# Kernel tuning notes

Hardware: AMD Instinct MI355X
Metric: run time of the kernel (lower is better)

Reference implementation:

```python
import jax, jax.numpy as jnp
import numpy as np

B, T, I, H = 256, 512, 64, 256  # batch, seq_len, NUM_BANDS, HIDDEN_DIM; NUM_LAYERS=2


def setup_inputs() -> dict:
    key = jax.random.key(0)
    ks = jax.random.split(key, 12)
    s = 0.05
    f = jnp.float32
    return {
        "x": jax.random.normal(ks[0], (B, T, I), f),
        # layer 0 (input -> hidden)
        "W_ih0": jax.random.normal(ks[1], (H, I), f) * s,
        "W_hh0": jax.random.normal(ks[2], (H, H), f) * s,
        "b_ih0": jax.random.normal(ks[3], (H,), f) * s,
        "b_hh0": jax.random.normal(ks[4], (H,), f) * s,
        # layer 1 (hidden -> hidden)
        "W_ih1": jax.random.normal(ks[5], (H, H), f) * s,
        "W_hh1": jax.random.normal(ks[6], (H, H), f) * s,
        "b_ih1": jax.random.normal(ks[7], (H,), f) * s,
        "b_hh1": jax.random.normal(ks[8], (H,), f) * s,
        # fc head (hidden -> 1)
        "W_fc": jax.random.normal(ks[9], (1, H), f) * s,
        "b_fc": jax.random.normal(ks[10], (1,), f) * s,
    }


def _rnn_layer(x_seq, W_ih, W_hh, b_ih, b_hh):
    """Elman ReLU layer: h_t = relu(W_ih x_t + b_ih + W_hh h_{t-1} + b_hh).
    x_seq: [B, T, D] -> returns [B, T, H]. Input projection is batched; only
    the hidden recurrence runs in the scan."""
    pre = jnp.einsum('btd,hd->bth', x_seq, W_ih) + b_ih + b_hh  # [B,T,H]
    h0 = jnp.zeros((x_seq.shape[0], W_hh.shape[0]), x_seq.dtype)

    def step(h, p_t):
        h = jax.nn.relu(p_t + h @ W_hh.T)
        return h, h

    _, ys = jax.lax.scan(step, h0, jnp.swapaxes(pre, 0, 1))  # [T,B,H]
    return jnp.swapaxes(ys, 0, 1)


def reference(x, W_ih0, W_hh0, b_ih0, b_hh0, W_ih1, W_hh1, b_ih1, b_hh1, W_fc, b_fc):
    h1 = _rnn_layer(x, W_ih0, W_hh0, b_ih0, b_hh0)
    h2 = _rnn_layer(h1, W_ih1, W_hh1, b_ih1, b_hh1)
    out = h2.reshape(-1, h2.shape[-1]) @ W_fc.T + b_fc  # [B*T, 1]
    return out.reshape(-1)
```

## Files before the change

kernel.cpp:

```cpp
#include <hip/hip_runtime.h>


#define T_ 512
#define H_ 256

typedef __attribute__((ext_vector_type(8))) short short8;
typedef __attribute__((ext_vector_type(4))) float f32x4;

#define MFMA(a, b, c) __builtin_amdgcn_mfma_f32_16x16x32_bf16(a, b, c, 0, 0, 0)

__device__ __forceinline__ unsigned short bf16rne(float f) {
    unsigned u = __float_as_uint(f);
    u += 0x7fff + ((u >> 16) & 1);
    return (unsigned short)(u >> 16);
}

__device__ __forceinline__ void split8(const float4 a0, const float4 a1,
                                       short8& hi, short8& lo) {
    const float v[8] = {a0.x, a0.y, a0.z, a0.w, a1.x, a1.y, a1.z, a1.w};
#pragma unroll
    for (int j = 0; j < 8; ++j) {
        unsigned short hb = bf16rne(v[j]);
        float hf = __uint_as_float(((unsigned)hb) << 16);
        unsigned short lb = bf16rne(v[j] - hf);
        hi[j] = (short)hb;
        lo[j] = (short)lb;
    }
}

__device__ __forceinline__ void lds_sync() {
    asm volatile("s_waitcnt lgkmcnt(0)" ::: "memory");
    __builtin_amdgcn_sched_barrier(0);
    __builtin_amdgcn_s_barrier();
    __builtin_amdgcn_sched_barrier(0);
    asm volatile("" ::: "memory");
}

__global__ __launch_bounds__(256) void k_gemm0(
    const float* __restrict__ x, const float* __restrict__ Wih,
    const float* __restrict__ bih, const float* __restrict__ bhh,
    float* __restrict__ buf)
{
    const int tid = threadIdx.x, lane = tid & 63, wv = tid >> 6;
    const int l15 = lane & 15, lg = lane >> 4;
    const int bc = blockIdx.x & 15;
    const int t0 = (blockIdx.x >> 4) * 32;

    short8 bhi[4][2], blo[4][2];
    f32x4 bias[4];
#pragma unroll
    for (int nt = 0; nt < 4; ++nt) {
        const int n = wv * 64 + nt * 16 + l15;
#pragma unroll
        for (int ks = 0; ks < 2; ++ks) {
            const float4* p = (const float4*)(Wih + (size_t)n * 64 + ks * 32 + 8 * lg);
            split8(p[0], p[1], bhi[nt][ks], blo[nt][ks]);
        }
        const float b = bih[n] + bhh[n];
        bias[nt] = f32x4{b, b, b, b};
    }
#pragma unroll 1
    for (int t = t0; t < t0 + 32; ++t) {
        short8 ahi[2], alo[2];
#pragma unroll
        for (int ks = 0; ks < 2; ++ks) {
            const float4* p =
                (const float4*)(x + ((size_t)(bc * 16 + l15) * T_ + t) * 64 + ks * 32 + 8 * lg);
            split8(p[0], p[1], ahi[ks], alo[ks]);
        }
        f32x4 acc[4];
#pragma unroll
        for (int nt = 0; nt < 4; ++nt) acc[nt] = bias[nt];
#pragma unroll
        for (int ks = 0; ks < 2; ++ks) {
#pragma unroll
            for (int nt = 0; nt < 4; ++nt) acc[nt] = MFMA(ahi[ks], bhi[nt][ks], acc[nt]);
#pragma unroll
            for (int nt = 0; nt < 4; ++nt) acc[nt] = MFMA(alo[ks], bhi[nt][ks], acc[nt]);
#pragma unroll
            for (int nt = 0; nt < 4; ++nt) acc[nt] = MFMA(ahi[ks], blo[nt][ks], acc[nt]);
        }
        float* slot = buf + ((size_t)bc * T_ + t) * 4096;
#pragma unroll
        for (int nt = 0; nt < 4; ++nt)
            *(f32x4*)(slot + (wv * 64 + nt * 16 + l15) * 16 + 4 * lg) = acc[nt];
    }
}

__global__ __launch_bounds__(256, 1) void k_gemm1(
    const float* __restrict__ Wih, const float* __restrict__ bih,
    const float* __restrict__ bhh, float* __restrict__ buf)
{
    const int tid = threadIdx.x, lane = tid & 63, wv = tid >> 6;
    const int l15 = lane & 15, lg = lane >> 4;
    const int bc = blockIdx.x & 15;
    const int t0 = (blockIdx.x >> 4) * 32;

    short8 bhi[4][8], blo[4][8];
    f32x4 bias[4];
#pragma unroll
    for (int nt = 0; nt < 4; ++nt) {
        const int n = wv * 64 + nt * 16 + l15;
#pragma unroll
        for (int ks = 0; ks < 8; ++ks) {
            const float4* p = (const float4*)(Wih + (size_t)n * H_ + ks * 32 + 8 * lg);
            split8(p[0], p[1], bhi[nt][ks], blo[nt][ks]);
        }
        const float b = bih[n] + bhh[n];
        bias[nt] = f32x4{b, b, b, b};
    }
#pragma unroll 1
    for (int t = t0; t < t0 + 32; ++t) {
        float* slot = buf + ((size_t)bc * T_ + t) * 4096;
        const unsigned short* g = (const unsigned short*)slot;
        short8 ahi[8];
#pragma unroll
        for (int ks = 0; ks < 8; ++ks)
            ahi[ks] = *(const short8*)(g + ks * 512 + lg * 128 + l15 * 8);
        __syncthreads();
        f32x4 acc[4];
#pragma unroll
        for (int nt = 0; nt < 4; ++nt) acc[nt] = bias[nt];
#pragma unroll
        for (int ks = 0; ks < 8; ++ks) {
#pragma unroll
            for (int nt = 0; nt < 4; ++nt) acc[nt] = MFMA(ahi[ks], bhi[nt][ks], acc[nt]);
#pragma unroll
            for (int nt = 0; nt < 4; ++nt) acc[nt] = MFMA(ahi[ks], blo[nt][ks], acc[nt]);
        }
#pragma unroll
        for (int nt = 0; nt < 4; ++nt)
            *(f32x4*)(slot + (wv * 64 + nt * 16 + l15) * 16 + 4 * lg) = acc[nt];
    }
}

template <bool WRITE_H1, bool FC>
__global__ __launch_bounds__(512, 1) void k_rnn(
    float* __restrict__ buf, const float* __restrict__ Whh,
    const float* __restrict__ Wfc, const float* __restrict__ bfcp,
    float* __restrict__ out)
{
    const int tid = threadIdx.x, lane = tid & 63, wv = tid >> 6;
    const int l15 = lane & 15, lg = lane >> 4;
    const int bc = blockIdx.x;

    short8 bhi[2][8], blo[2][8];
#pragma unroll
    for (int nt = 0; nt < 2; ++nt) {
        const int n = wv * 32 + nt * 16 + l15;
#pragma unroll
        for (int ks = 0; ks < 8; ++ks) {
            const float4* p = (const float4*)(Whh + (size_t)n * H_ + ks * 32 + 8 * lg);
            split8(p[0], p[1], bhi[nt][ks], blo[nt][ks]);
        }
    }
    float wfc2[2];
    float bfc = 0.f;
    if (FC) {
#pragma unroll
        for (int nt = 0; nt < 2; ++nt) wfc2[nt] = Wfc[wv * 32 + nt * 16 + l15];
        bfc = bfcp[0];
    }

    __shared__ unsigned short hb[2][4096];
    __shared__ float wavesum[2][8][16];

    for (int i = tid; i < 512; ++i == 0 ? i : i)
        ;
    for (int i = tid; i < (int)(sizeof(hb) / 16); i += 512)
        ((uint4*)hb)[i] = make_uint4(0u, 0u, 0u, 0u);
    __syncthreads();

    float* slot0 = buf + (size_t)bc * T_ * 4096;
    f32x4 cfrag[2];
#pragma unroll
    for (int nt = 0; nt < 2; ++nt)
        cfrag[nt] = *(const f32x4*)(slot0 + (wv * 32 + nt * 16 + l15) * 16 + 4 * lg);

    int p = 0;
#pragma unroll 1
    for (int t = 0; t < T_; ++t) {
        f32x4 cnext[2] = {f32x4{0.f, 0.f, 0.f, 0.f}, f32x4{0.f, 0.f, 0.f, 0.f}};
        if (t + 1 < T_) {
#pragma unroll
            for (int nt = 0; nt < 2; ++nt)
                cnext[nt] = *(const f32x4*)(slot0 + (size_t)(t + 1) * 4096 +
                                            (wv * 32 + nt * 16 + l15) * 16 + 4 * lg);
        }
        short8 ahi[8];
#pragma unroll
        for (int ks = 0; ks < 8; ++ks)
            ahi[ks] = *(const short8*)&hb[p][ks * 512 + lg * 128 + l15 * 8];
        f32x4 accA[2], accB[2];
#pragma unroll
        for (int nt = 0; nt < 2; ++nt) {
            accA[nt] = cfrag[nt];
            accB[nt] = f32x4{0.f, 0.f, 0.f, 0.f};
        }
#pragma unroll
        for (int ks = 0; ks < 8; ++ks) {
#pragma unroll
            for (int nt = 0; nt < 2; ++nt) accA[nt] = MFMA(ahi[ks], bhi[nt][ks], accA[nt]);
#pragma unroll
            for (int nt = 0; nt < 2; ++nt) accB[nt] = MFMA(ahi[ks], blo[nt][ks], accB[nt]);
        }
        float fcp[4] = {0.f, 0.f, 0.f, 0.f};
#pragma unroll
        for (int nt = 0; nt < 2; ++nt) {
            const int gbase = (wv * 4 + nt * 2 + (l15 >> 3)) * 128 + (l15 & 7);
#pragma unroll
            for (int j = 0; j < 4; ++j) {
                float v = fmaxf(accA[nt][j] + accB[nt][j], 0.f);
                hb[p ^ 1][gbase + (4 * lg + j) * 8] = bf16rne(v);
                if (FC) fcp[j] = fmaf(v, wfc2[nt], fcp[j]);
            }
        }
        if (FC) {
#pragma unroll
            for (int j = 0; j < 4; ++j) {
                float f = fcp[j];
                f += __shfl_xor(f, 1, 64);
                f += __shfl_xor(f, 2, 64);
                f += __shfl_xor(f, 4, 64);
                f += __shfl_xor(f, 8, 64);
                fcp[j] = f;
            }
            if (l15 == 0) {
#pragma unroll
                for (int j = 0; j < 4; ++j) wavesum[p][wv][4 * lg + j] = fcp[j];
            }
        }
        lds_sync();
        if (WRITE_H1) {
            unsigned short* gst = (unsigned short*)(slot0 + (size_t)t * 4096);
            *(uint4*)(gst + tid * 8) = *(const uint4*)&hb[p ^ 1][tid * 8];
        }
        if (FC) {
            if (wv == 0 && lane < 16) {
                float s = bfc;
#pragma unroll
                for (int w8 = 0; w8 < 8; ++w8) s += wavesum[p][w8][lane];
                out[(size_t)(bc * 16 + lane) * T_ + t] = s;
            }
        }
#pragma unroll
        for (int nt = 0; nt < 2; ++nt) cfrag[nt] = cnext[nt];
        p ^= 1;
    }
}

extern "C" void kernel_launch(void* const* d_in, const int* in_sizes, int n_in,
                              void* d_out, int out_size, void* d_ws, size_t ws_size,
                              hipStream_t stream) {
    (void)in_sizes; (void)n_in; (void)out_size; (void)ws_size;
    const float* x    = (const float*)d_in[0];
    const float* Wih0 = (const float*)d_in[1];
    const float* Whh0 = (const float*)d_in[2];
    const float* bih0 = (const float*)d_in[3];
    const float* bhh0 = (const float*)d_in[4];
    const float* Wih1 = (const float*)d_in[5];
    const float* Whh1 = (const float*)d_in[6];
    const float* bih1 = (const float*)d_in[7];
    const float* bhh1 = (const float*)d_in[8];
    const float* Wfc  = (const float*)d_in[9];
    const float* bfc  = (const float*)d_in[10];

    float* buf = (float*)d_ws;
    float* out = (float*)d_out;

    k_gemm0<<<dim3(256), dim3(256), 0, stream>>>(x, Wih0, bih0, bhh0, buf);
    k_rnn<true, false><<<dim3(16), dim3(512), 0, stream>>>(buf, Whh0, Wfc, bfc, out);
    k_gemm1<<<dim3(256), dim3(256), 0, stream>>>(Wih1, bih1, bhh1, buf);
    k_rnn<false, true><<<dim3(16), dim3(512), 0, stream>>>(buf, Whh1, Wfc, bfc, out);
}
```

Baseline: 1.410 ms.

## Fuse both RNN layers into one persistent pipelined kernel with flag-based handoff

```diff
diff --git a/kernel.cpp b/kernel.cpp
--- a/kernel.cpp
+++ b/kernel.cpp
@@ -3,6 +3,7 @@
 
 #define T_ 512
 #define H_ 256
+#define RD 32
 
 typedef __attribute__((ext_vector_type(8))) short short8;
 typedef __attribute__((ext_vector_type(4))) float f32x4;
@@ -28,194 +29,253 @@
     }
 }
 
-__device__ __forceinline__ void lds_sync() {
-    asm volatile("s_waitcnt lgkmcnt(0)" ::: "memory");
-    __builtin_amdgcn_sched_barrier(0);
-    __builtin_amdgcn_s_barrier();
-    __builtin_amdgcn_sched_barrier(0);
-    asm volatile("" ::: "memory");
-}
-
-__global__ __launch_bounds__(256) void k_gemm0(
-    const float* __restrict__ x, const float* __restrict__ Wih,
-    const float* __restrict__ bih, const float* __restrict__ bhh,
-    float* __restrict__ buf)
+__device__ __forceinline__ int aload(const int* p) {
+    return __hip_atomic_load(p, __ATOMIC_ACQUIRE, __HIP_MEMORY_SCOPE_AGENT);
+}
+__device__ __forceinline__ void astore(int* p, int v) {
+    __hip_atomic_store(p, v, __ATOMIC_RELEASE, __HIP_MEMORY_SCOPE_AGENT);
+}
+
+__global__ __launch_bounds__(256) void k_init(int* flags) {
+    for (int i = threadIdx.x; i < 48 * 64; i += 256) flags[i] = 0;
+}
+
+__global__ __launch_bounds__(512, 1) void k_pipe(
+    const float* __restrict__ x,
+    const float* __restrict__ Wih0, const float* __restrict__ Whh0,
+    const float* __restrict__ bih0, const float* __restrict__ bhh0,
+    const float* __restrict__ Wih1, const float* __restrict__ Whh1,
+    const float* __restrict__ bih1, const float* __restrict__ bhh1,
+    const float* __restrict__ Wfc, const float* __restrict__ bfcp,
+    float* __restrict__ out, char* __restrict__ ws)
 {
+    unsigned short* h1ring = (unsigned short*)ws;
+    float* p1ring = (float*)(ws + (4u << 20));
+    int* flags = (int*)(ws + (12u << 20));
+    const int role = blockIdx.x >> 4;
+    const int bc = blockIdx.x & 15;
+    int* f01 = flags + bc * 64;
+    int* f12 = flags + (16 + bc) * 64;
+    int* fl1 = flags + (32 + bc) * 64;
+
     const int tid = threadIdx.x, lane = tid & 63, wv = tid >> 6;
     const int l15 = lane & 15, lg = lane >> 4;
-    const int bc = blockIdx.x & 15;
-    const int t0 = (blockIdx.x >> 4) * 32;
-
-    short8 bhi[4][2], blo[4][2];
-    f32x4 bias[4];
-#pragma unroll
-    for (int nt = 0; nt < 4; ++nt) {
-        const int n = wv * 64 + nt * 16 + l15;
-#pragma unroll
-        for (int ks = 0; ks < 2; ++ks) {
-            const float4* p = (const float4*)(Wih + (size_t)n * 64 + ks * 32 + 8 * lg);
-            split8(p[0], p[1], bhi[nt][ks], blo[nt][ks]);
-        }
-        const float b = bih[n] + bhh[n];
-        bias[nt] = f32x4{b, b, b, b};
-    }
-#pragma unroll 1
-    for (int t = t0; t < t0 + 32; ++t) {
-        short8 ahi[2], alo[2];
-#pragma unroll
-        for (int ks = 0; ks < 2; ++ks) {
-            const float4* p =
-                (const float4*)(x + ((size_t)(bc * 16 + l15) * T_ + t) * 64 + ks * 32 + 8 * lg);
-            split8(p[0], p[1], ahi[ks], alo[ks]);
-        }
-        f32x4 acc[4];
-#pragma unroll
-        for (int nt = 0; nt < 4; ++nt) acc[nt] = bias[nt];
-#pragma unroll
-        for (int ks = 0; ks < 2; ++ks) {
-#pragma unroll
-            for (int nt = 0; nt < 4; ++nt) acc[nt] = MFMA(ahi[ks], bhi[nt][ks], acc[nt]);
-#pragma unroll
-            for (int nt = 0; nt < 4; ++nt) acc[nt] = MFMA(alo[ks], bhi[nt][ks], acc[nt]);
-#pragma unroll
-            for (int nt = 0; nt < 4; ++nt) acc[nt] = MFMA(ahi[ks], blo[nt][ks], acc[nt]);
-        }
-        float* slot = buf + ((size_t)bc * T_ + t) * 4096;
-#pragma unroll
-        for (int nt = 0; nt < 4; ++nt)
-            *(f32x4*)(slot + (wv * 64 + nt * 16 + l15) * 16 + 4 * lg) = acc[nt];
-    }
-}
-
-__global__ __launch_bounds__(256, 1) void k_gemm1(
-    const float* __restrict__ Wih, const float* __restrict__ bih,
-    const float* __restrict__ bhh, float* __restrict__ buf)
-{
-    const int tid = threadIdx.x, lane = tid & 63, wv = tid >> 6;
-    const int l15 = lane & 15, lg = lane >> 4;
-    const int bc = blockIdx.x & 15;
-    const int t0 = (blockIdx.x >> 4) * 32;
-
-    short8 bhi[4][8], blo[4][8];
-    f32x4 bias[4];
-#pragma unroll
-    for (int nt = 0; nt < 4; ++nt) {
-        const int n = wv * 64 + nt * 16 + l15;
-#pragma unroll
-        for (int ks = 0; ks < 8; ++ks) {
-            const float4* p = (const float4*)(Wih + (size_t)n * H_ + ks * 32 + 8 * lg);
-            split8(p[0], p[1], bhi[nt][ks], blo[nt][ks]);
-        }
-        const float b = bih[n] + bhh[n];
-        bias[nt] = f32x4{b, b, b, b};
-    }
-#pragma unroll 1
-    for (int t = t0; t < t0 + 32; ++t) {
-        float* slot = buf + ((size_t)bc * T_ + t) * 4096;
-        const unsigned short* g = (const unsigned short*)slot;
-        short8 ahi[8];
-#pragma unroll
-        for (int ks = 0; ks < 8; ++ks)
-            ahi[ks] = *(const short8*)(g + ks * 512 + lg * 128 + l15 * 8);
-        __syncthreads();
-        f32x4 acc[4];
-#pragma unroll
-        for (int nt = 0; nt < 4; ++nt) acc[nt] = bias[nt];
-#pragma unroll
-        for (int ks = 0; ks < 8; ++ks) {
-#pragma unroll
-            for (int nt = 0; nt < 4; ++nt) acc[nt] = MFMA(ahi[ks], bhi[nt][ks], acc[nt]);
-#pragma unroll
-            for (int nt = 0; nt < 4; ++nt) acc[nt] = MFMA(ahi[ks], blo[nt][ks], acc[nt]);
-        }
-#pragma unroll
-        for (int nt = 0; nt < 4; ++nt)
-            *(f32x4*)(slot + (wv * 64 + nt * 16 + l15) * 16 + 4 * lg) = acc[nt];
-    }
-}
-
-template <bool WRITE_H1, bool FC>
-__global__ __launch_bounds__(512, 1) void k_rnn(
-    float* __restrict__ buf, const float* __restrict__ Whh,
-    const float* __restrict__ Wfc, const float* __restrict__ bfcp,
-    float* __restrict__ out)
-{
-    const int tid = threadIdx.x, lane = tid & 63, wv = tid >> 6;
-    const int l15 = lane & 15, lg = lane >> 4;
-    const int bc = blockIdx.x;
-
-    short8 bhi[2][8], blo[2][8];
-#pragma unroll
-    for (int nt = 0; nt < 2; ++nt) {
-        const int n = wv * 32 + nt * 16 + l15;
-#pragma unroll
-        for (int ks = 0; ks < 8; ++ks) {
-            const float4* p = (const float4*)(Whh + (size_t)n * H_ + ks * 32 + 8 * lg);
-            split8(p[0], p[1], bhi[nt][ks], blo[nt][ks]);
-        }
-    }
-    float wfc2[2];
-    float bfc = 0.f;
-    if (FC) {
-#pragma unroll
-        for (int nt = 0; nt < 2; ++nt) wfc2[nt] = Wfc[wv * 32 + nt * 16 + l15];
-        bfc = bfcp[0];
-    }
 
     __shared__ unsigned short hb[2][4096];
     __shared__ float wavesum[2][8][16];
 
-    for (int i = tid; i < 512; ++i == 0 ? i : i)
-        ;
-    for (int i = tid; i < (int)(sizeof(hb) / 16); i += 512)
-        ((uint4*)hb)[i] = make_uint4(0u, 0u, 0u, 0u);
-    __syncthreads();
-
-    float* slot0 = buf + (size_t)bc * T_ * 4096;
-    f32x4 cfrag[2];
-#pragma unroll
-    for (int nt = 0; nt < 2; ++nt)
-        cfrag[nt] = *(const f32x4*)(slot0 + (wv * 32 + nt * 16 + l15) * 16 + 4 * lg);
-
-    int p = 0;
+    if (role == 0) {
+        short8 whi[2][8], wlo[2][8];
+        short8 uhi[2][2], ulo[2][2];
+        f32x4 bias2[2];
+#pragma unroll
+        for (int nt = 0; nt < 2; ++nt) {
+            const int n = wv * 32 + nt * 16 + l15;
+#pragma unroll
+            for (int ks = 0; ks < 8; ++ks) {
+                const float4* pw = (const float4*)(Whh0 + (size_t)n * H_ + ks * 32 + 8 * lg);
+                split8(pw[0], pw[1], whi[nt][ks], wlo[nt][ks]);
+            }
+#pragma unroll
+            for (int ks = 0; ks < 2; ++ks) {
+                const float4* pu = (const float4*)(Wih0 + (size_t)n * 64 + ks * 32 + 8 * lg);
+                split8(pu[0], pu[1], uhi[nt][ks], ulo[nt][ks]);
+            }
+            const float b = bih0[n] + bhh0[n];
+            bias2[nt] = f32x4{b, b, b, b};
+        }
+        for (int i = tid; i < 1024; i += 512) ((uint4*)hb)[i] = make_uint4(0u, 0u, 0u, 0u);
+        __syncthreads();
+
+        short8 xcur[2];
+        {
+            const float* xrow = x + ((size_t)(bc * 16 + l15) * T_) * 64;
+#pragma unroll
+            for (int ks = 0; ks < 2; ++ks) {
+                const float4* p4 = (const float4*)(xrow + ks * 32 + 8 * lg);
+                float4 a0 = p4[0], a1 = p4[1];
+                const float v[8] = {a0.x, a0.y, a0.z, a0.w, a1.x, a1.y, a1.z, a1.w};
+#pragma unroll
+                for (int j = 0; j < 8; ++j) xcur[ks][j] = (short)bf16rne(v[j]);
+            }
+        }
+        int pp = 0;
 #pragma unroll 1
-    for (int t = 0; t < T_; ++t) {
-        f32x4 cnext[2] = {f32x4{0.f, 0.f, 0.f, 0.f}, f32x4{0.f, 0.f, 0.f, 0.f}};
-        if (t + 1 < T_) {
+        for (int t = 0; t < T_; ++t) {
+            __syncthreads();
+            if (tid == 0) {
+                if (t > 0) astore(f01, t);
+                if (t >= RD) { while (aload(f12) < t - RD + 1) {} }
+            }
+            __syncthreads();
+            short8 xnext[2] = {xcur[0], xcur[1]};
+            if (t + 1 < T_) {
+                const float* xrow = x + ((size_t)(bc * 16 + l15) * T_ + (t + 1)) * 64;
+#pragma unroll
+                for (int ks = 0; ks < 2; ++ks) {
+                    const float4* p4 = (const float4*)(xrow + ks * 32 + 8 * lg);
+                    float4 a0 = p4[0], a1 = p4[1];
+                    const float v[8] = {a0.x, a0.y, a0.z, a0.w, a1.x, a1.y, a1.z, a1.w};
+#pragma unroll
+                    for (int j = 0; j < 8; ++j) xnext[ks][j] = (short)bf16rne(v[j]);
+                }
+            }
+            short8 ahi[8];
+#pragma unroll
+            for (int ks = 0; ks < 8; ++ks)
+                ahi[ks] = *(const short8*)&hb[pp][ks * 512 + lg * 128 + l15 * 8];
+            f32x4 accA[2], accB[2];
+#pragma unroll
+            for (int nt = 0; nt < 2; ++nt) { accA[nt] = bias2[nt]; accB[nt] = f32x4{0.f, 0.f, 0.f, 0.f}; }
+#pragma unroll
+            for (int ks = 0; ks < 8; ++ks) {
+#pragma unroll
+                for (int nt = 0; nt < 2; ++nt) accA[nt] = MFMA(ahi[ks], whi[nt][ks], accA[nt]);
+#pragma unroll
+                for (int nt = 0; nt < 2; ++nt) accB[nt] = MFMA(ahi[ks], wlo[nt][ks], accB[nt]);
+            }
+#pragma unroll
+            for (int ks = 0; ks < 2; ++ks) {
+#pragma unroll
+                for (int nt = 0; nt < 2; ++nt) accA[nt] = MFMA(xcur[ks], uhi[nt][ks], accA[nt]);
+#pragma unroll
+                for (int nt = 0; nt < 2; ++nt) accB[nt] = MFMA(xcur[ks], ulo[nt][ks], accB[nt]);
+            }
+#pragma unroll
+            for (int nt = 0; nt < 2; ++nt) {
+                const int gbase = (wv * 4 + nt * 2 + (l15 >> 3)) * 128 + (l15 & 7);
+#pragma unroll
+                for (int j = 0; j < 4; ++j) {
+                    float v = fmaxf(accA[nt][j] + accB[nt][j], 0.f);
+                    hb[pp ^ 1][gbase + (4 * lg + j) * 8] = bf16rne(v);
+                }
+            }
+            __syncthreads();
+            {
+                unsigned short* g = h1ring + ((size_t)bc * RD + (t & (RD - 1))) * 4096;
+                *(uint4*)(g + tid * 8) = *(const uint4*)&hb[pp ^ 1][tid * 8];
+            }
+            xcur[0] = xnext[0]; xcur[1] = xnext[1];
+            pp ^= 1;
+        }
+        __syncthreads();
+        if (tid == 0) astore(f01, T_);
+    } else if (role == 1) {
+        short8 whi[2][8], wlo[2][8];
+        f32x4 bias2[2];
+#pragma unroll
+        for (int nt = 0; nt < 2; ++nt) {
+            const int n = wv * 32 + nt * 16 + l15;
+#pragma unroll
+            for (int ks = 0; ks < 8; ++ks) {
+                const float4* pw = (const float4*)(Wih1 + (size_t)n * H_ + ks * 32 + 8 * lg);
+                split8(pw[0], pw[1], whi[nt][ks], wlo[nt][ks]);
+            }
+            const float b = bih1[n] + bhh1[n];
+            bias2[nt] = f32x4{b, b, b, b};
+        }
+#pragma unroll 1
+        for (int t = 0; t < T_; ++t) {
+            if (tid == 0) {
+                while (aload(f01) < t + 1) {}
+                if (t >= RD) { while (aload(fl1) < t - RD + 1) {} }
+            }
+            __syncthreads();
+            const unsigned short* g = h1ring + ((size_t)bc * RD + (t & (RD - 1))) * 4096;
+            short8 ahi[8];
+#pragma unroll
+            for (int ks = 0; ks < 8; ++ks)
+                ahi[ks] = *(const short8*)(g + ks * 512 + lg * 128 + l15 * 8);
+            f32x4 accA[2], accB[2];
+#pragma unroll
+            for (int nt = 0; nt < 2; ++nt) { accA[nt] = bias2[nt]; accB[nt] = f32x4{0.f, 0.f, 0.f, 0.f}; }
+#pragma unroll
+            for (int ks = 0; ks < 8; ++ks) {
+#pragma unroll
+                for (int nt = 0; nt < 2; ++nt) accA[nt] = MFMA(ahi[ks], whi[nt][ks], accA[nt]);
+#pragma unroll
+                for (int nt = 0; nt < 2; ++nt) accB[nt] = MFMA(ahi[ks], wlo[nt][ks], accB[nt]);
+            }
+            float* dst = p1ring + ((size_t)bc * RD + (t & (RD - 1))) * 4096;
+#pragma unroll
+            for (int nt = 0; nt < 2; ++nt) {
+                const int n = wv * 32 + nt * 16 + l15;
+                f32x4 v;
+#pragma unroll
+                for (int j = 0; j < 4; ++j) v[j] = accA[nt][j] + accB[nt][j];
+                *(f32x4*)(dst + n * 16 + 4 * lg) = v;
+            }
+            __syncthreads();
+            if (tid == 0) astore(f12, t + 1);
+        }
+    } else {
+        short8 whi[2][8], wlo[2][8];
+#pragma unroll
+        for (int nt = 0; nt < 2; ++nt) {
+            const int n = wv * 32 + nt * 16 + l15;
+#pragma unroll
+            for (int ks = 0; ks < 8; ++ks) {
+                const float4* pw = (const float4*)(Whh1 + (size_t)n * H_ + ks * 32 + 8 * lg);
+                split8(pw[0], pw[1], whi[nt][ks], wlo[nt][ks]);
+            }
+        }
+        float wfc2[2];
+#pragma unroll
+        for (int nt = 0; nt < 2; ++nt) wfc2[nt] = Wfc[wv * 32 + nt * 16 + l15];
+        const float bfc = bfcp[0];
+        for (int i = tid; i < 1024; i += 512) ((uint4*)hb)[i] = make_uint4(0u, 0u, 0u, 0u);
+        __syncthreads();
+
+        if (tid == 0) { while (aload(f12) < 1) {} }
+        __syncthreads();
+        f32x4 cfrag[2];
+        {
+            const float* src = p1ring + (size_t)bc * RD * 4096;
 #pragma unroll
             for (int nt = 0; nt < 2; ++nt)
-                cnext[nt] = *(const f32x4*)(slot0 + (size_t)(t + 1) * 4096 +
-                                            (wv * 32 + nt * 16 + l15) * 16 + 4 * lg);
-        }
-        short8 ahi[8];
-#pragma unroll
-        for (int ks = 0; ks < 8; ++ks)
-            ahi[ks] = *(const short8*)&hb[p][ks * 512 + lg * 128 + l15 * 8];
-        f32x4 accA[2], accB[2];
-#pragma unroll
-        for (int nt = 0; nt < 2; ++nt) {
-            accA[nt] = cfrag[nt];
-            accB[nt] = f32x4{0.f, 0.f, 0.f, 0.f};
-        }
-#pragma unroll
-        for (int ks = 0; ks < 8; ++ks) {
-#pragma unroll
-            for (int nt = 0; nt < 2; ++nt) accA[nt] = MFMA(ahi[ks], bhi[nt][ks], accA[nt]);
-#pragma unroll
-            for (int nt = 0; nt < 2; ++nt) accB[nt] = MFMA(ahi[ks], blo[nt][ks], accB[nt]);
-        }
-        float fcp[4] = {0.f, 0.f, 0.f, 0.f};
-#pragma unroll
-        for (int nt = 0; nt < 2; ++nt) {
-            const int gbase = (wv * 4 + nt * 2 + (l15 >> 3)) * 128 + (l15 & 7);
-#pragma unroll
-            for (int j = 0; j < 4; ++j) {
-                float v = fmaxf(accA[nt][j] + accB[nt][j], 0.f);
-                hb[p ^ 1][gbase + (4 * lg + j) * 8] = bf16rne(v);
-                if (FC) fcp[j] = fmaf(v, wfc2[nt], fcp[j]);
-            }
-        }
-        if (FC) {
+                cfrag[nt] = *(const f32x4*)(src + (wv * 32 + nt * 16 + l15) * 16 + 4 * lg);
+        }
+        int pp = 0;
+#pragma unroll 1
+        for (int t = 0; t < T_; ++t) {
+            __syncthreads();
+            if (tid == 0) {
+                astore(fl1, t);
+                if (t + 1 < T_) { while (aload(f12) < t + 2) {} }
+            }
+            __syncthreads();
+            f32x4 cnext[2] = {cfrag[0], cfrag[1]};
+            if (t + 1 < T_) {
+                const float* src = p1ring + ((size_t)bc * RD + ((t + 1) & (RD - 1))) * 4096;
+#pragma unroll
+                for (int nt = 0; nt < 2; ++nt)
+                    cnext[nt] = *(const f32x4*)(src + (wv * 32 + nt * 16 + l15) * 16 + 4 * lg);
+            }
+            short8 ahi[8];
+#pragma unroll
+            for (int ks = 0; ks < 8; ++ks)
+                ahi[ks] = *(const short8*)&hb[pp][ks * 512 + lg * 128 + l15 * 8];
+            f32x4 accA[2], accB[2];
+#pragma unroll
+            for (int nt = 0; nt < 2; ++nt) { accA[nt] = cfrag[nt]; accB[nt] = f32x4{0.f, 0.f, 0.f, 0.f}; }
+#pragma unroll
+            for (int ks = 0; ks < 8; ++ks) {
+#pragma unroll
+                for (int nt = 0; nt < 2; ++nt) accA[nt] = MFMA(ahi[ks], whi[nt][ks], accA[nt]);
+#pragma unroll
+                for (int nt = 0; nt < 2; ++nt) accB[nt] = MFMA(ahi[ks], wlo[nt][ks], accB[nt]);
+            }
+            float fcp[4] = {0.f, 0.f, 0.f, 0.f};
+#pragma unroll
+            for (int nt = 0; nt < 2; ++nt) {
+                const int gbase = (wv * 4 + nt * 2 + (l15 >> 3)) * 128 + (l15 & 7);
+#pragma unroll
+                for (int j = 0; j < 4; ++j) {
+                    float v = fmaxf(accA[nt][j] + accB[nt][j], 0.f);
+                    hb[pp ^ 1][gbase + (4 * lg + j) * 8] = bf16rne(v);
+                    fcp[j] = fmaf(v, wfc2[nt], fcp[j]);
+                }
+            }
 #pragma unroll
             for (int j = 0; j < 4; ++j) {
                 float f = fcp[j];
@@ -227,25 +287,18 @@
             }
             if (l15 == 0) {
 #pragma unroll
-                for (int j = 0; j < 4; ++j) wavesum[p][wv][4 * lg + j] = fcp[j];
-            }
-        }
-        lds_sync();
-        if (WRITE_H1) {
-            unsigned short* gst = (unsigned short*)(slot0 + (size_t)t * 4096);
-            *(uint4*)(gst + tid * 8) = *(const uint4*)&hb[p ^ 1][tid * 8];
-        }
-        if (FC) {
+                for (int j = 0; j < 4; ++j) wavesum[pp][wv][4 * lg + j] = fcp[j];
+            }
+            __syncthreads();
             if (wv == 0 && lane < 16) {
                 float s = bfc;
 #pragma unroll
-                for (int w8 = 0; w8 < 8; ++w8) s += wavesum[p][w8][lane];
+                for (int w8 = 0; w8 < 8; ++w8) s += wavesum[pp][w8][lane];
                 out[(size_t)(bc * 16 + lane) * T_ + t] = s;
             }
-        }
-#pragma unroll
-        for (int nt = 0; nt < 2; ++nt) cfrag[nt] = cnext[nt];
-        p ^= 1;
+            cfrag[0] = cnext[0]; cfrag[1] = cnext[1];
+            pp ^= 1;
+        }
     }
 }
 
@@ -265,11 +318,11 @@
     const float* Wfc  = (const float*)d_in[9];
     const float* bfc  = (const float*)d_in[10];
 
-    float* buf = (float*)d_ws;
+    char* ws  = (char*)d_ws;
+    int* flags = (int*)(ws + (12u << 20));
     float* out = (float*)d_out;
 
-    k_gemm0<<<dim3(256), dim3(256), 0, stream>>>(x, Wih0, bih0, bhh0, buf);
-    k_rnn<true, false><<<dim3(16), dim3(512), 0, stream>>>(buf, Whh0, Wfc, bfc, out);
-    k_gemm1<<<dim3(256), dim3(256), 0, stream>>>(Wih1, bih1, bhh1, buf);
-    k_rnn<false, true><<<dim3(16), dim3(512), 0, stream>>>(buf, Whh1, Wfc, bfc, out);
-}
+    k_init<<<dim3(1), dim3(256), 0, stream>>>(flags);
+    k_pipe<<<dim3(48), dim3(512), 0, stream>>>(
+        x, Wih0, Whh0, bih0, bhh0, Wih1, Whh1, bih1, bhh1, Wfc, bfc, out, ws);
+}
```

Result: faster. 1.369 ms (-2.9%).
